# Kernel tuning notes

Measured on AMD Instinct MI355X. Metric: run time of the kernel, lower is better.

Reference implementation:

```python
import jax, jax.numpy as jnp
import numpy as np
from jax.scipy.special import erf

Z = 87
NREF = 7
NC = 5
NW = 23
N_ATOMS = 75000
N_PAIRS = 1500000
BOHR = 0.5291772105638411
HARTREE = 27.211386024367243
K4, K5, K6, KK = 4.10451, 19.08857, 254.5553148552, 7.5
E3 = float(np.exp(3.0))

def _sp_inv(x):
    # inverse of softplus, so that softplus(raw) == x
    return float(np.log(np.expm1(x)))

def compute_refc6(scale_q_raw, refsys, zeff, refh, sscale, secaiw, gam, ascale, alphaiw, hcount, cpw):
    # gather per-reference-system atomic data via refsys indices [Z, NREF]
    zeff_r = zeff[refsys][..., None]
    sscale_r = sscale[refsys][..., None]
    secaiw_r = secaiw[refsys]            # [Z, NREF, NW]
    gam_r = gam[refsys][..., None]
    refh_i = refh[..., None] * jax.nn.softplus(scale_q_raw)[0]
    qmod = zeff_r + refh_i
    qsafe = jnp.where(qmod > 1e-8, qmod, 1.0)
    zfac = jnp.where(qmod > 1e-8, jnp.exp(3.0 * (1.0 - jnp.exp(2.0 * gam_r * (1.0 - zeff_r / qsafe)))), E3)
    alpha = sscale_r * secaiw_r * zfac
    alpha = jnp.maximum(ascale[..., None] * (alphaiw - hcount[..., None] * alpha), 0.0)  # [Z, NREF, NW]
    # Casimir-Polder integration: refc6[i,j,a,b] = 3/(2pi) * sum_w alpha[i,a,w]*alpha[j,b,w]*w
    return (3.0 / (2.0 * np.pi)) * jnp.einsum('iaw,jbw,w->ijab', alpha, alpha, cpw)

def _forward(species, edge_index, lengths, partial_charges, s6_raw, s8_raw, a1_raw, a2_raw, scale_q_raw, refsys, zeff, refh, sscale, secaiw, gam, ascale, alphaiw, hcount, cpw, rcov, en, ncount_mask, ncount_weight, cn, fixgweights, refq, sqrt_r4r2):
    n = species.shape[0]
    idx_i, idx_j = edge_index[0], edge_index[1]
    r = lengths * (1.0 / BOHR)
    sp_i, sp_j = species[idx_i], species[idx_j]
    # erf-based coordination number
    rcov_ij = (4.0 / 3.0) * (rcov[sp_i] + rcov[sp_j])
    den = K4 * jnp.exp(-((jnp.abs(en[sp_i] - en[sp_j]) + K5) ** 2) / K6)
    countf = den * 0.5 * (1.0 + erf(-KK * (r - rcov_ij) / rcov_ij))
    ncoord = jax.ops.segment_sum(countf, idx_i, num_segments=n)  # [N]
    # Gaussian reference weights over (NREF, NC)
    nce = ncoord[:, None, None]
    gw = jnp.exp(-6.0 * ncount_weight[species] * (nce - cn[species]) ** 2)
    gw = jnp.sum(ncount_mask[species] * gw, axis=-1)  # [N, NREF]
    norm = jnp.clip(jnp.sum(gw, axis=-1, keepdims=True), 1e-7, None)
    gw = jnp.where(norm > 1e-8, gw / norm, fixgweights[species])
    # charge scaling zeta
    spq = jax.nn.softplus(scale_q_raw)[0]
    zeff_s = zeff[species][:, None]
    qref = zeff_s + refq[species] * spq
    qmod = zeff_s + partial_charges[:, None]
    qsafe = jnp.where(qmod > 1e-8, qmod, 1.0)
    zeta = jnp.where(qmod > 1e-8, jnp.exp(3.0 * (1.0 - jnp.exp(2.0 * gam[species][:, None] * (1.0 - qref / qsafe)))), E3) * gw  # [N, NREF]
    # pairwise C6 via reference C6 table
    refc6 = compute_refc6(scale_q_raw, refsys, zeff, refh, sscale, secaiw, gam, ascale, alphaiw, hcount, cpw)
    c6 = jnp.einsum('pab,pa,pb->p', refc6[sp_i, sp_j], zeta[idx_i], zeta[idx_j])  # [P]
    # Becke-Johnson damped -C6/r^6 - C8/r^8
    r4r2 = 3.0 * sqrt_r4r2[sp_i] * sqrt_r4r2[sp_j]
    a1 = jax.nn.softplus(a1_raw)[0]
    a2 = jax.nn.softplus(a2_raw)[0]
    s6 = jax.nn.softplus(s6_raw)[0]
    s8 = jax.nn.softplus(s8_raw)[0]
    r0sq = (a1 * jnp.sqrt(r4r2) + a2) ** 2
    r2 = r * r
    r6 = r2 * r2 * r2
    r8 = r6 * r2
    pair = -c6 * (s6 / (r6 + r0sq ** 3) + s8 * r4r2 / (r8 + r0sq ** 4))
    # per-atom dispersion energy in eV (0.5 because each pair counted twice in edge list)
    return 0.5 * HARTREE * jax.ops.segment_sum(pair, idx_i, num_segments=n)

def setup_inputs():
    key = jax.random.key(0)
    ks = jax.random.split(key, 24)
    u = lambda k, sh, lo, hi: jax.random.uniform(k, sh, jnp.float32, lo, hi)
    return {
        'species': jax.random.randint(ks[0], (N_ATOMS,), 0, Z),
        'edge_index': jax.random.randint(ks[1], (2, N_PAIRS), 0, N_ATOMS),
        'lengths': u(ks[2], (N_PAIRS,), 1.5, 6.0),
        'partial_charges': 0.1 * jax.random.normal(ks[3], (N_ATOMS,), jnp.float32),
        's6_raw': jnp.array([_sp_inv(1.0)], jnp.float32),
        's8_raw': jnp.array([_sp_inv(1.61679827)], jnp.float32),
        'a1_raw': jnp.array([_sp_inv(0.44959224)], jnp.float32),
        'a2_raw': jnp.array([_sp_inv(3.35743605)], jnp.float32),
        'scale_q_raw': jnp.array([_sp_inv(1.0)], jnp.float32),
        'refsys': jax.random.randint(ks[4], (Z, NREF), 0, Z),
        'zeff': u(ks[5], (Z,), 1.0, 10.0),
        'refh': u(ks[6], (Z, NREF), -0.5, 0.5),
        'sscale': u(ks[7], (Z,), 0.5, 1.5),
        'secaiw': u(ks[8], (Z, NW), 0.1, 5.0),
        'gam': u(ks[9], (Z,), 0.1, 0.5),
        'ascale': u(ks[10], (Z, NREF), 0.5, 1.5),
        'alphaiw': u(ks[11], (Z, NREF, NW), 0.5, 20.0),
        'hcount': u(ks[12], (Z, NREF), 0.0, 3.0),
        'cpw': u(ks[13], (NW,), 0.01, 0.5),
        'rcov': u(ks[14], (Z,), 0.5, 3.0),
        'en': u(ks[15], (Z,), 0.8, 4.0),
        'ncount_mask': (jax.random.uniform(ks[16], (Z, NREF, NC)) > 0.5).astype(jnp.float32),
        'ncount_weight': u(ks[17], (Z, NREF, NC), 0.5, 2.0),
        'cn': u(ks[18], (Z, NREF, NC), 0.0, 6.0),
        'fixgweights': jnp.full((Z, NREF), 1.0 / NREF, jnp.float32),
        'refq': u(ks[19], (Z, NREF), -0.5, 0.5),
        'sqrt_r4r2': u(ks[20], (Z,), 2.0, 10.0),
    }

def reference(species, edge_index, lengths, partial_charges, s6_raw, s8_raw, a1_raw, a2_raw, scale_q_raw, refsys, zeff, refh, sscale, secaiw, gam, ascale, alphaiw, hcount, cpw, rcov, en, ncount_mask, ncount_weight, cn, fixgweights, refq, sqrt_r4r2):
    return _forward(species, edge_index, lengths, partial_charges, s6_raw, s8_raw, a1_raw, a2_raw, scale_q_raw, refsys, zeff, refh, sscale, secaiw, gam, ascale, alphaiw, hcount, cpw, rcov, en, ncount_mask, ncount_weight, cn, fixgweights, refq, sqrt_r4r2)
```

## Files before the change

kernel.cpp:

```cpp
#include <hip/hip_runtime.h>
#include <hip/hip_bf16.h>
#include <hip/hip_fp16.h>

#define ZZ      87
#define NREF    7
#define NC      5
#define NW      23
#define NATOMS  75000
#define NPAIRS  1500000
#define IAW     (ZZ*NREF*NW)

#define BSH     7
#define BSZ     128
#define NB      586
#define BLKP    4096
#define NBLK    367
#define PREP_BLKS 147
#define PACK_BLKS 22

#define OFF_ALPHA   32
#define OFF_AD      14040
#define OFF_NCOORD  164040
#define OFF_ENERGY  239040
#define OFF_IMG     OFF_ENERGY
#define OFF_BETA    314048
#define OFF_HIST    1214048
#define OFF_BTOT    1643586
#define OFF_BBASE   1644176
#define OFF_REC     1644768
#define SORT_WS_NEED      ((size_t)(OFF_REC + 2*NPAIRS) * 4)

#define IMG_A   0
#define IMG_C   7308
#define IMG_Q   13398
#define IMG_G   14008
#define IMG_DW  14356

static constexpr float INV_BOHR  = (float)(1.0/0.5291772105638411);
static constexpr float HALF_HART = (float)(0.5*27.211386024367243);
static constexpr float CK4 = 4.10451f;
static constexpr float CK5 = 19.08857f;
static constexpr float INV_K6 = (float)(1.0/254.5553148552);
static constexpr float CKK = 7.5f;
static constexpr float E3F = 20.085536923187668f;
static constexpr float C32PI = 0.47746482927568606f;

__device__ __forceinline__ bool detect_bf16(const void* s6raw) {
    return ((*(const unsigned short*)s6raw) >> 8) == 0x3Fu;
}
__device__ __forceinline__ float ldf(const void* p, int i, bool bf) {
    if (bf) {
        unsigned int u = ((const unsigned short*)p)[i];
        return __uint_as_float(u << 16);
    }
    return ((const float*)p)[i];
}
__device__ __forceinline__ float splus(float x) {
    return (x > 15.f) ? x : log1pf(expf(x));
}
__device__ __forceinline__ void up2(unsigned int u, float* d) {
    __half2 h;
    *reinterpret_cast<unsigned int*>(&h) = u;
    float2 f = __half22float2(h);
    d[0] = f.x; d[1] = f.y;
}
__device__ __forceinline__ void unpack24(uint4 a, uint4 b, uint4 c, float* v) {
    up2(a.x, v+0);  up2(a.y, v+2);  up2(a.z, v+4);  up2(a.w, v+6);
    up2(b.x, v+8);  up2(b.y, v+10); up2(b.z, v+12); up2(b.w, v+14);
    up2(c.x, v+16); up2(c.y, v+18); up2(c.z, v+20); up2(c.w, v+22);
}
__device__ __forceinline__ void ld8(const void* p, int p0, bool bf, float* L) {
    if (bf) {
        uint4 u = *(const uint4*)((const unsigned short*)p + p0);
        unsigned vs[4] = {u.x, u.y, u.z, u.w};
        #pragma unroll
        for (int k = 0; k < 4; ++k) {
            L[2*k]   = __uint_as_float(vs[k] << 16);
            L[2*k+1] = __uint_as_float(vs[k] & 0xFFFF0000u);
        }
    } else {
        float4 f0 = *(const float4*)((const float*)p + p0);
        float4 f1 = *(const float4*)((const float*)p + p0 + 4);
        L[0]=f0.x; L[1]=f0.y; L[2]=f0.z; L[3]=f0.w;
        L[4]=f1.x; L[5]=f1.y; L[6]=f1.z; L[7]=f1.w;
    }
}

__device__ __forceinline__ void prep_body(int t, bool bf,
        const int* __restrict__ refsys, const int* __restrict__ species,
        const void* zeff, const void* refh, const void* sscale,
        const void* secaiw, const void* gam, const void* ascale,
        const void* alphaiw, const void* hcount, const void* cpw,
        const void* rcov, const void* en,
        const void* s6r, const void* s8r, const void* a1r,
        const void* a2r, const void* sqr, float* __restrict__ ws) {
    if (t == 0) {
        ws[0] = splus(ldf(sqr, 0, bf));
        ws[1] = splus(ldf(s6r, 0, bf));
        ws[2] = splus(ldf(s8r, 0, bf));
        ws[3] = splus(ldf(a1r, 0, bf));
        ws[4] = splus(ldf(a2r, 0, bf));
    }
    if (t < NATOMS) {
        int sp = species[t];
        ((float2*)(ws + OFF_AD))[t] = make_float2(ldf(rcov, sp, bf), ldf(en, sp, bf));
    }
    if (t >= IAW) return;
    int w  = t % NW;
    int ia = t / NW;
    int rs = refsys[ia];
    float spq  = splus(ldf(sqr, 0, bf));
    float ze   = ldf(zeff, rs, bf);
    float qmod = ze + ldf(refh, ia, bf) * spq;
    float zfac;
    if (qmod > 1e-8f) {
        float g = ldf(gam, rs, bf);
        zfac = expf(3.f * (1.f - expf(2.f * g * (1.f - ze / qmod))));
    } else {
        zfac = E3F;
    }
    float sec = ldf(sscale, rs, bf) * ldf(secaiw, rs*NW + w, bf) * zfac;
    float al  = ldf(ascale, ia, bf) *
                (ldf(alphaiw, ia*NW + w, bf) - ldf(hcount, ia, bf) * sec);
    float bsw = sqrtf(C32PI * ldf(cpw, w, bf));
    ws[OFF_ALPHA + t] = fmaxf(al, 0.f) * bsw;
}


__global__ __launch_bounds__(512) void k_prep_hist(
        const int* __restrict__ refsys, const int* __restrict__ species,
        const void* zeff, const void* refh, const void* sscale,
        const void* secaiw, const void* gam, const void* ascale,
        const void* alphaiw, const void* hcount, const void* cpw,
        const void* rcov, const void* en,
        const void* s6r, const void* s8r, const void* a1r,
        const void* a2r, const void* sqr,
        const int* __restrict__ eidx, int* __restrict__ hist,
        float* __restrict__ ws) {
    const bool bf = detect_bf16(s6r);
    __shared__ int h[NB];
    int blk = blockIdx.x;
    if (blk < PREP_BLKS) {
        prep_body(blk * 512 + (int)threadIdx.x, bf, refsys, species, zeff, refh,
                  sscale, secaiw, gam, ascale, alphaiw, hcount, cpw, rcov, en,
                  s6r, s8r, a1r, a2r, sqr, ws);
        return;
    }
    int hb = blk - PREP_BLKS;
    for (int t = threadIdx.x; t < NB; t += 512) h[t] = 0;
    __syncthreads();
    int p0 = hb * BLKP + (int)threadIdx.x * 8;
    if (p0 + 8 <= NPAIRS) {
        int4 a0 = *(const int4*)(eidx + p0);
        int4 a1 = *(const int4*)(eidx + p0 + 4);
        atomicAdd(&h[a0.x >> BSH], 1);
        atomicAdd(&h[a0.y >> BSH], 1);
        atomicAdd(&h[a0.z >> BSH], 1);
        atomicAdd(&h[a0.w >> BSH], 1);
        atomicAdd(&h[a1.x >> BSH], 1);
        atomicAdd(&h[a1.y >> BSH], 1);
        atomicAdd(&h[a1.z >> BSH], 1);
        atomicAdd(&h[a1.w >> BSH], 1);
    }
    __syncthreads();
    for (int t = threadIdx.x; t < NB; t += 512)
        hist[(size_t)hb * NB + t] = h[t];
}

__global__ __launch_bounds__(1024) void k_scan_bucket(int* __restrict__ hist,
                                                      int* __restrict__ btot) {
    int b = blockIdx.x;
    int t = threadIdx.x;
    int v = (t < NBLK) ? hist[(size_t)t * NB + b] : 0;
    int lane = t & 63, wid = t >> 6;
    int x = v;
    #pragma unroll
    for (int d = 1; d < 64; d <<= 1) {
        int n = __shfl_up(x, d, 64);
        if (lane >= d) x += n;
    }
    __shared__ int wsum[16];
    if (lane == 63) wsum[wid] = x;
    __syncthreads();
    if (t == 0) {
        int acc = 0;
        #pragma unroll
        for (int w = 0; w < 16; ++w) { int s = wsum[w]; wsum[w] = acc; acc += s; }
    }
    __syncthreads();
    int incl = x + wsum[wid];
    if (t < NBLK) hist[(size_t)t * NB + b] = incl - v;
    if (t == 1023) btot[b] = incl;
}

__global__ __launch_bounds__(1024) void k_scan_base(const int* __restrict__ btot,
                                                    int* __restrict__ bbase) {
    int t = threadIdx.x;
    int v = (t < NB) ? btot[t] : 0;
    int lane = t & 63, wid = t >> 6;
    int x = v;
    #pragma unroll
    for (int d = 1; d < 64; d <<= 1) {
        int n = __shfl_up(x, d, 64);
        if (lane >= d) x += n;
    }
    __shared__ int wsum[16];
    if (lane == 63) wsum[wid] = x;
    __syncthreads();
    if (t == 0) {
        int acc = 0;
        #pragma unroll
        for (int w = 0; w < 16; ++w) { int s = wsum[w]; wsum[w] = acc; acc += s; }
    }
    __syncthreads();
    int incl = x + wsum[wid];
    if (t < NB) bbase[t] = incl - v;
    if (t == 1023) bbase[NB] = incl;
}

__global__ __launch_bounds__(512) void k_scatter_pack(
        const int* __restrict__ eidx, const void* lengths, const void* s6r,
        const int* __restrict__ hist, const int* __restrict__ bbase,
        uint2* __restrict__ rec,
        const void* zeff, const void* gam, const void* mask,
        const void* wght, const void* cn, const void* refq, const void* sq4,
        float* __restrict__ ws) {
    const bool bf = detect_bf16(s6r);
    __shared__ int cnt[NB];
    int blk = blockIdx.x;
    if (blk >= NBLK) {
        unsigned* img = (unsigned*)(ws + OFF_IMG);
        int t = (blk - NBLK) * 512 + (int)threadIdx.x;
        if (t < 7308) {
            int row = t / 12, u = t % 12;
            int w0 = 2*u, w1 = 2*u + 1;
            const float* aF = ws + OFF_ALPHA + row * NW;
            float v0 = aF[w0];
            float v1 = (w1 < NW) ? aF[w1] : 0.f;
            unsigned lo = __half_as_ushort(__float2half(v0));
            unsigned hi = __half_as_ushort(__float2half(v1));
            img[t] = lo | (hi << 16);
        } else if (t < 7308 + 3045) {
            int e = t - 7308;
            float cnv = ldf(cn, e, bf);
            float wv  = (ldf(mask, e, bf) > 0.5f) ? ldf(wght, e, bf) : -1.f;
            ((float2*)(img + IMG_C))[e] = make_float2(cnv, wv);
        } else if (t < 10353 + 609) {
            int e = t - 10353;
            int sp = e / NREF;
            ((float*)(img + IMG_Q))[e] = ldf(zeff, sp, bf) + ldf(refq, e, bf) * ws[0];
        } else if (t < 10962 + 87) {
            int sp = t - 10962;
            ((float4*)(img + IMG_G))[sp] = make_float4(ldf(zeff, sp, bf),
                                                       ldf(gam, sp, bf),
                                                       ldf(sq4, sp, bf), 0.f);
        } else if (t == 11049) {
            img[14007] = 0;
        }
        return;
    }
    const int* hcol = hist + (size_t)blk * NB;
    for (int t = threadIdx.x; t < NB; t += 512)
        cnt[t] = bbase[t] + hcol[t];
    __syncthreads();
    int p0 = blk * BLKP + (int)threadIdx.x * 8;
    if (p0 + 8 > NPAIRS) return;
    int4 a0 = *(const int4*)(eidx + p0);
    int4 a1 = *(const int4*)(eidx + p0 + 4);
    int4 b0 = *(const int4*)(eidx + NPAIRS + p0);
    int4 b1 = *(const int4*)(eidx + NPAIRS + p0 + 4);
    float L[8];
    ld8(lengths, p0, bf, L);
    int is[8] = {a0.x,a0.y,a0.z,a0.w,a1.x,a1.y,a1.z,a1.w};
    int js[8] = {b0.x,b0.y,b0.z,b0.w,b1.x,b1.y,b1.z,b1.w};
    #pragma unroll
    for (int k = 0; k < 8; ++k) {
        int b = is[k] >> BSH;
        int pos = atomicAdd(&cnt[b], 1);
        rec[pos] = make_uint2(((unsigned)(is[k] & (BSZ-1)) << 17) | (unsigned)js[k],
                              __float_as_uint(L[k]));
    }
}

__global__ __launch_bounds__(512) void k_ncbeta(const uint2* __restrict__ rec,
        const int* __restrict__ bbase, const int* __restrict__ species,
        const void* pq, const void* s6r, float* __restrict__ ws) {
    const bool bf = detect_bf16(s6r);
    __shared__ __align__(16) unsigned s_img[IMG_DW];
    __shared__ float bins[BSZ];
    __shared__ float adl[BSZ * 2];
    int b = blockIdx.x;
    int a0 = b << BSH;
    int na = NATOMS - a0; if (na > BSZ) na = BSZ;
    {
        const uint4* g4 = (const uint4*)(ws + OFF_IMG);
        uint4* s4 = (uint4*)s_img;
        for (int t = threadIdx.x; t < IMG_DW/4; t += 512) s4[t] = g4[t];
    }
    for (int t = threadIdx.x; t < BSZ; t += 512) bins[t] = 0.f;
    const float2* AD = (const float2*)(ws + OFF_AD);
    for (int t = threadIdx.x; t < na; t += 512) {
        float2 v = AD[a0 + t];
        adl[2*t] = v.x; adl[2*t + 1] = v.y;
    }
    __syncthreads();
    int bs = bbase[b], be = bbase[b + 1];
    for (int p = bs + (int)threadIdx.x; p < be; p += 2*512) {
        int p2 = p + 512;
        bool h2 = (p2 < be);
        uint2 r1 = rec[p];
        uint2 r2 = h2 ? rec[p2] : r1;
        int il1 = (r1.x >> 17) & (BSZ-1), j1 = r1.x & 0x1FFFF;
        int il2 = (r2.x >> 17) & (BSZ-1), j2 = r2.x & 0x1FFFF;
        float2 aj1 = AD[j1];
        float2 aj2 = AD[j2];
        {
            float r  = __uint_as_float(r1.y) * INV_BOHR;
            float rc = (4.f/3.f) * (adl[2*il1] + aj1.x);
            float d  = fabsf(adl[2*il1+1] - aj1.y) + CK5;
            float cf = CK4 * expf(-(d*d)*INV_K6) * 0.5f * (1.f + erff(-CKK*(r-rc)/rc));
            atomicAdd(&bins[il1], cf);
        }
        if (h2) {
            float r  = __uint_as_float(r2.y) * INV_BOHR;
            float rc = (4.f/3.f) * (adl[2*il2] + aj2.x);
            float d  = fabsf(adl[2*il2+1] - aj2.y) + CK5;
            float cf = CK4 * expf(-(d*d)*INV_K6) * 0.5f * (1.f + erff(-CKK*(r-rc)/rc));
            atomicAdd(&bins[il2], cf);
        }
    }
    __syncthreads();
    int t = threadIdx.x;
    if (t >= na) return;
    int k = a0 + t;
    const unsigned* sA = s_img;
    const float2*   sC = (const float2*)(s_img + IMG_C);
    const float*    sQ = (const float*)(s_img + IMG_Q);
    const float4*   sG = (const float4*)(s_img + IMG_G);

    int sp = species[k];
    float nce = bins[t];
    float4 zg = sG[sp];
    float qmod = zg.x + ldf(pq, k, bf);

    float gw[NREF];
    float sum = 0.f;
    #pragma unroll
    for (int a = 0; a < NREF; ++a) {
        float g = 0.f;
        #pragma unroll
        for (int c = 0; c < NC; ++c) {
            float2 cw = sC[sp*35 + a*NC + c];
            float dlt = nce - cw.x;
            float e = __expf(-6.f * cw.y * dlt * dlt);
            g += (cw.y > 0.f) ? e : 0.f;
        }
        gw[a] = g; sum += g;
    }
    float inv = 1.f / fmaxf(sum, 1e-7f);

    float2 acc[12];
    #pragma unroll
    for (int u = 0; u < 12; ++u) acc[u] = make_float2(0.f, 0.f);
    #pragma unroll
    for (int a = 0; a < NREF; ++a) {
        float qref = sQ[sp*NREF + a];
        float zf = (qmod > 1e-8f)
                 ? __expf(3.f * (1.f - __expf(2.f * zg.y * (1.f - qref / qmod))))
                 : E3F;
        float za = zf * gw[a] * inv;
        const uint2* ar = (const uint2*)(sA + (sp*NREF + a) * 12);
        #pragma unroll
        for (int u2 = 0; u2 < 6; ++u2) {
            uint2 h = ar[u2];
            float f[4];
            up2(h.x, f); up2(h.y, f+2);
            acc[2*u2].x   = fmaf(f[0], za, acc[2*u2].x);
            acc[2*u2].y   = fmaf(f[1], za, acc[2*u2].y);
            acc[2*u2+1].x = fmaf(f[2], za, acc[2*u2+1].x);
            acc[2*u2+1].y = fmaf(f[3], za, acc[2*u2+1].y);
        }
    }
    alignas(16) __half hrow[24];
    #pragma unroll
    for (int u = 0; u < 12; ++u) {
        hrow[2*u]   = __float2half(acc[u].x);
        hrow[2*u+1] = __float2half(acc[u].y);
    }
    hrow[23] = __float2half(zg.z);
    uint4* dst = (uint4*)((char*)(ws + OFF_BETA) + (size_t)k * 48);
    const uint4* src = (const uint4*)hrow;
    dst[0] = src[0]; dst[1] = src[1]; dst[2] = src[2];
}

__device__ __forceinline__ float pair_energy(const float* vi, const float* vj,
                                             float len, float s6, float s8,
                                             float a1, float a2) {
    float c6 = 0.f;
    #pragma unroll
    for (int w = 0; w < NW; ++w) c6 = fmaf(vi[w], vj[w], c6);
    float rr = 3.f * vi[23] * vj[23];
    float r  = len * INV_BOHR;
    float r2 = r * r;
    float r6 = r2 * r2 * r2;
    float r8 = r6 * r2;
    float r0   = a1 * sqrtf(rr) + a2;
    float r0sq = r0 * r0;
    float r0_6 = r0sq * r0sq * r0sq;
    float r0_8 = r0_6 * r0sq;
    return -c6 * (s6 / (r6 + r0_6) + s8 * rr / (r8 + r0_8));
}

__global__ __launch_bounds__(512) void k_energy_s(const uint2* __restrict__ rec,
        const int* __restrict__ bbase, const float* __restrict__ ws,
        void* __restrict__ out, const void* s6r) {
    const bool bf = detect_bf16(s6r);
    __shared__ float bins[BSZ];
    __shared__ unsigned irow[BSZ * 13];
    int b = blockIdx.x;
    int a0 = b << BSH;
    int na = NATOMS - a0; if (na > BSZ) na = BSZ;
    for (int t = threadIdx.x; t < BSZ; t += 512) bins[t] = 0.f;
    const unsigned* betaU = (const unsigned*)(ws + OFF_BETA);
    for (int t = threadIdx.x; t < na * 12; t += 512) {
        int l = t / 12, k = t - l * 12;
        irow[l * 13 + k] = betaU[(size_t)(a0 + l) * 12 + k];
    }
    __syncthreads();
    float s6 = ws[1], s8 = ws[2], a1 = ws[3], a2 = ws[4];
    int bs = bbase[b], be = bbase[b + 1];
    const char* B = (const char*)betaU;
    for (int p = bs + (int)threadIdx.x; p < be; p += 2*512) {
        int p2 = p + 512;
        bool h2 = (p2 < be);
        uint2 r1 = rec[p];
        uint2 r2 = h2 ? rec[p2] : r1;
        int il1 = (r1.x >> 17) & (BSZ-1), j1 = r1.x & 0x1FFFF;
        int il2 = (r2.x >> 17) & (BSZ-1), j2 = r2.x & 0x1FFFF;
        const uint4* J1 = (const uint4*)(B + (size_t)j1 * 48);
        const uint4* J2 = (const uint4*)(B + (size_t)j2 * 48);
        uint4 ja0 = J1[0], ja1 = J1[1], ja2 = J1[2];
        uint4 jb0 = J2[0], jb1 = J2[1], jb2 = J2[2];
        float vi[24], vj[24];
        #pragma unroll
        for (int k = 0; k < 12; ++k) up2(irow[il1*13 + k], vi + 2*k);
        unpack24(ja0, ja1, ja2, vj);
        float e1 = pair_energy(vi, vj, __uint_as_float(r1.y), s6, s8, a1, a2);
        atomicAdd(&bins[il1], e1);
        if (h2) {
            #pragma unroll
            for (int k = 0; k < 12; ++k) up2(irow[il2*13 + k], vi + 2*k);
            unpack24(jb0, jb1, jb2, vj);
            float e2 = pair_energy(vi, vj, __uint_as_float(r2.y), s6, s8, a1, a2);
            atomicAdd(&bins[il2], e2);
        }
    }
    __syncthreads();
    for (int t = threadIdx.x; t < na; t += 512) {
        float v = HALF_HART * bins[t];
        if (bf) ((__hip_bfloat16*)out)[a0 + t] = __float2bfloat16(v);
        else    ((float*)out)[a0 + t] = v;
    }
}


__global__ void k_prep_fb(const int* __restrict__ refsys, const int* __restrict__ species,
                          const void* zeff, const void* refh, const void* sscale,
                          const void* secaiw, const void* gam, const void* ascale,
                          const void* alphaiw, const void* hcount, const void* cpw,
                          const void* rcov, const void* en,
                          const void* s6r, const void* s8r, const void* a1r,
                          const void* a2r, const void* sqr,
                          float* __restrict__ ws) {
    const bool bf = detect_bf16(s6r);
    prep_body(blockIdx.x * blockDim.x + threadIdx.x, bf, refsys, species, zeff,
              refh, sscale, secaiw, gam, ascale, alphaiw, hcount, cpw, rcov, en,
              s6r, s8r, a1r, a2r, sqr, ws);
}

__device__ __forceinline__ float2 ldf2(const void* p, int t, bool bf) {
    if (bf) {
        unsigned int u = ((const unsigned int*)p)[t];
        return make_float2(__uint_as_float(u << 16),
                           __uint_as_float(u & 0xFFFF0000u));
    }
    return ((const float2*)p)[t];
}

__global__ void k_ncoord_fb(const int* __restrict__ eidx, const void* lengths,
                            const void* s6r, float* __restrict__ ws) {
    const bool bf = detect_bf16(s6r);
    int t = blockIdx.x * blockDim.x + threadIdx.x;
    if (2*t >= NPAIRS) return;
    int2 ii = ((const int2*)eidx)[t];
    int2 jj = ((const int2*)(eidx + NPAIRS))[t];
    float2 L = ldf2(lengths, t, bf);
    const float2* AD = (const float2*)(ws + OFF_AD);
    float2 ai = AD[ii.x], aj = AD[jj.x];
    float2 bi = AD[ii.y], bj = AD[jj.y];
    float r0  = L.x * INV_BOHR;
    float rc0 = (4.f/3.f) * (ai.x + aj.x);
    float d0  = fabsf(ai.y - aj.y) + CK5;
    float cf0 = CK4 * expf(-(d0*d0) * INV_K6) * 0.5f * (1.f + erff(-CKK * (r0 - rc0) / rc0));
    float r1  = L.y * INV_BOHR;
    float rc1 = (4.f/3.f) * (bi.x + bj.x);
    float d1  = fabsf(bi.y - bj.y) + CK5;
    float cf1 = CK4 * expf(-(d1*d1) * INV_K6) * 0.5f * (1.f + erff(-CKK * (r1 - rc1) / rc1));
    atomicAdd(ws + OFF_NCOORD + ii.x, cf0);
    atomicAdd(ws + OFF_NCOORD + ii.y, cf1);
}

__global__ void k_beta_fb(const int* __restrict__ species, const void* pq,
                          const void* zeff, const void* gam,
                          const void* mask, const void* wght, const void* cn,
                          const void* refq, const void* sq4, const void* s6r,
                          float* __restrict__ ws) {
    const bool bf = detect_bf16(s6r);
    int k = blockIdx.x * blockDim.x + threadIdx.x;
    if (k >= NATOMS) return;
    int sp = species[k];
    float nce = ws[OFF_NCOORD + k];
    float spq = ws[0];
    float gw[NREF];
    float sum = 0.f;
    #pragma unroll
    for (int a = 0; a < NREF; ++a) {
        float g = 0.f;
        #pragma unroll
        for (int c = 0; c < NC; ++c) {
            int idx = (sp*NREF + a)*NC + c;
            float dlt = nce - ldf(cn, idx, bf);
            g += ldf(mask, idx, bf) * expf(-6.f * ldf(wght, idx, bf) * dlt * dlt);
        }
        gw[a] = g; sum += g;
    }
    float inv  = 1.f / fmaxf(sum, 1e-7f);
    float ze   = ldf(zeff, sp, bf);
    float qmod = ze + ldf(pq, k, bf);
    float gm   = ldf(gam, sp, bf);
    float beta[NW];
    #pragma unroll
    for (int w = 0; w < NW; ++w) beta[w] = 0.f;
    const float* A = ws + OFF_ALPHA + sp * (NREF*NW);
    #pragma unroll
    for (int a = 0; a < NREF; ++a) {
        float qref = ze + ldf(refq, sp*NREF + a, bf) * spq;
        float zf = (qmod > 1e-8f)
                 ? expf(3.f * (1.f - expf(2.f * gm * (1.f - qref / qmod))))
                 : E3F;
        float za = zf * gw[a] * inv;
        #pragma unroll
        for (int w = 0; w < NW; ++w) beta[w] = fmaf(A[a*NW + w], za, beta[w]);
    }
    alignas(16) __half hrow[24];
    #pragma unroll
    for (int w = 0; w < NW; ++w) hrow[w] = __float2half(beta[w]);
    hrow[23] = __float2half(ldf(sq4, sp, bf));
    uint4* dst = (uint4*)((char*)(ws + OFF_BETA) + (size_t)k * 48);
    const uint4* src = (const uint4*)hrow;
    dst[0] = src[0]; dst[1] = src[1]; dst[2] = src[2];
}

__global__ void k_energy_fb(const int* __restrict__ eidx, const void* lengths,
                            const void* s6r, float* __restrict__ ws) {
    const bool bf = detect_bf16(s6r);
    int t = blockIdx.x * blockDim.x + threadIdx.x;
    if (2*t >= NPAIRS) return;
    int2 ii = ((const int2*)eidx)[t];
    int2 jj = ((const int2*)(eidx + NPAIRS))[t];
    float2 L = ldf2(lengths, t, bf);
    const char* B = (const char*)(ws + OFF_BETA);
    const uint4* qi0 = (const uint4*)(B + (size_t)ii.x * 48);
    const uint4* qj0 = (const uint4*)(B + (size_t)jj.x * 48);
    const uint4* qi1 = (const uint4*)(B + (size_t)ii.y * 48);
    const uint4* qj1 = (const uint4*)(B + (size_t)jj.y * 48);
    uint4 ra0 = qi0[0], ra1 = qi0[1], ra2 = qi0[2];
    uint4 rb0 = qj0[0], rb1 = qj0[1], rb2 = qj0[2];
    uint4 rc0 = qi1[0], rc1 = qi1[1], rc2 = qi1[2];
    uint4 rd0 = qj1[0], rd1 = qj1[1], rd2 = qj1[2];
    float s6 = ws[1], s8 = ws[2], a1 = ws[3], a2 = ws[4];
    float vi[24], vj[24];
    unpack24(ra0, ra1, ra2, vi);
    unpack24(rb0, rb1, rb2, vj);
    float e0 = pair_energy(vi, vj, L.x, s6, s8, a1, a2);
    unpack24(rc0, rc1, rc2, vi);
    unpack24(rd0, rd1, rd2, vj);
    float e1 = pair_energy(vi, vj, L.y, s6, s8, a1, a2);
    atomicAdd(ws + OFF_ENERGY + ii.x, e0);
    atomicAdd(ws + OFF_ENERGY + ii.y, e1);
}

__global__ void k_final(const float* __restrict__ ws, void* out, const void* s6r) {
    const bool bf = detect_bf16(s6r);
    int k = blockIdx.x * blockDim.x + threadIdx.x;
    if (k >= NATOMS) return;
    float v = HALF_HART * ws[OFF_ENERGY + k];
    if (bf) ((__hip_bfloat16*)out)[k] = __float2bfloat16(v);
    else    ((float*)out)[k] = v;
}

extern "C" void kernel_launch(void* const* d_in, const int* in_sizes, int n_in,
                              void* d_out, int out_size, void* d_ws, size_t ws_size,
                              hipStream_t stream) {
    (void)in_sizes; (void)n_in; (void)out_size;

    const int*  species = (const int*)d_in[0];
    const int*  eidx    = (const int*)d_in[1];
    const void* lengths = d_in[2];
    const void* pq      = d_in[3];
    const void* s6r     = d_in[4];
    const void* s8r     = d_in[5];
    const void* a1r     = d_in[6];
    const void* a2r     = d_in[7];
    const void* sqr     = d_in[8];
    const int*  refsys  = (const int*)d_in[9];
    const void* zeff    = d_in[10];
    const void* refh    = d_in[11];
    const void* sscale  = d_in[12];
    const void* secaiw  = d_in[13];
    const void* gam     = d_in[14];
    const void* ascale  = d_in[15];
    const void* alphaiw = d_in[16];
    const void* hcount  = d_in[17];
    const void* cpw     = d_in[18];
    const void* rcov    = d_in[19];
    const void* en      = d_in[20];
    const void* mask    = d_in[21];
    const void* wght    = d_in[22];
    const void* cn      = d_in[23];
    const void* refq    = d_in[25];
    const void* sq4     = d_in[26];

    float* ws = (float*)d_ws;
    const bool use_sort = (ws_size >= SORT_WS_NEED);

    if (use_sort) {
        int*   hist  = (int*)(ws + OFF_HIST);
        int*   btot  = (int*)(ws + OFF_BTOT);
        int*   bbase = (int*)(ws + OFF_BBASE);
        uint2* rec   = (uint2*)(ws + OFF_REC);

        k_prep_hist  <<<PREP_BLKS + NBLK, 512, 0, stream>>>(refsys, species,
                         zeff, refh, sscale, secaiw, gam, ascale, alphaiw,
                         hcount, cpw, rcov, en, s6r, s8r, a1r, a2r, sqr,
                         eidx, hist, ws);
        k_scan_bucket<<<NB, 1024, 0, stream>>>(hist, btot);
        k_scan_base  <<<1,  1024, 0, stream>>>(btot, bbase);
        k_scatter_pack<<<NBLK + PACK_BLKS, 512, 0, stream>>>(eidx, lengths, s6r,
                         hist, bbase, rec, zeff, gam, mask, wght, cn, refq,
                         sq4, ws);
        k_ncbeta     <<<NB, 512, 0, stream>>>(rec, bbase, species, pq, s6r, ws);
        k_energy_s   <<<NB, 512, 0, stream>>>(rec, bbase, ws, d_out, s6r);
    } else {
        hipMemsetAsync(ws + OFF_NCOORD, 0, (size_t)(2 * NATOMS) * sizeof(float), stream);
        k_prep_fb  <<<(NATOMS   + 511)/512, 512, 0, stream>>>(refsys, species,
                        zeff, refh, sscale, secaiw, gam, ascale, alphaiw,
                        hcount, cpw, rcov, en, s6r, s8r, a1r, a2r, sqr, ws);
        k_ncoord_fb<<<(NPAIRS/2 + 255)/256, 256, 0, stream>>>(eidx, lengths, s6r, ws);
        k_beta_fb  <<<(NATOMS   + 255)/256, 256, 0, stream>>>(species, pq, zeff, gam,
                        mask, wght, cn, refq, sq4, s6r, ws);
        k_energy_fb<<<(NPAIRS/2 + 255)/256, 256, 0, stream>>>(eidx, lengths, s6r, ws);
        k_final    <<<(NATOMS   + 255)/256, 256, 0, stream>>>(ws, d_out, s6r);
    }
}
```

Measured before the change: 75.38 us.

## Fuse bucket and base scans via last-block ticket, move prep into scan kernel

```diff
diff --git a/kernel.cpp b/kernel.cpp
--- a/kernel.cpp
+++ b/kernel.cpp
@@ -15,9 +15,10 @@
 #define NB      586
 #define BLKP    4096
 #define NBLK    367
-#define PREP_BLKS 147
+#define PREPB   74
 #define PACK_BLKS 22
 
+#define OFF_DONE    8
 #define OFF_ALPHA   32
 #define OFF_AD      14040
 #define OFF_NCOORD  164040
@@ -127,29 +128,15 @@
 }
 
 
-__global__ __launch_bounds__(512) void k_prep_hist(
-        const int* __restrict__ refsys, const int* __restrict__ species,
-        const void* zeff, const void* refh, const void* sscale,
-        const void* secaiw, const void* gam, const void* ascale,
-        const void* alphaiw, const void* hcount, const void* cpw,
-        const void* rcov, const void* en,
-        const void* s6r, const void* s8r, const void* a1r,
-        const void* a2r, const void* sqr,
-        const int* __restrict__ eidx, int* __restrict__ hist,
-        float* __restrict__ ws) {
-    const bool bf = detect_bf16(s6r);
+__global__ __launch_bounds__(512) void k_hist(const int* __restrict__ eidx,
+                                              int* __restrict__ hist,
+                                              float* __restrict__ ws) {
     __shared__ int h[NB];
     int blk = blockIdx.x;
-    if (blk < PREP_BLKS) {
-        prep_body(blk * 512 + (int)threadIdx.x, bf, refsys, species, zeff, refh,
-                  sscale, secaiw, gam, ascale, alphaiw, hcount, cpw, rcov, en,
-                  s6r, s8r, a1r, a2r, sqr, ws);
-        return;
-    }
-    int hb = blk - PREP_BLKS;
+    if (blk == 0 && threadIdx.x == 0) ((int*)ws)[OFF_DONE] = 0;
     for (int t = threadIdx.x; t < NB; t += 512) h[t] = 0;
     __syncthreads();
-    int p0 = hb * BLKP + (int)threadIdx.x * 8;
+    int p0 = blk * BLKP + (int)threadIdx.x * 8;
     if (p0 + 8 <= NPAIRS) {
         int4 a0 = *(const int4*)(eidx + p0);
         int4 a1 = *(const int4*)(eidx + p0 + 4);
@@ -164,13 +151,31 @@
     }
     __syncthreads();
     for (int t = threadIdx.x; t < NB; t += 512)
-        hist[(size_t)hb * NB + t] = h[t];
-}
-
-__global__ __launch_bounds__(1024) void k_scan_bucket(int* __restrict__ hist,
-                                                      int* __restrict__ btot) {
-    int b = blockIdx.x;
+        hist[(size_t)blk * NB + t] = h[t];
+}
+
+__global__ __launch_bounds__(1024) void k_scan_prep(
+        int* __restrict__ hist, int* __restrict__ btot, int* __restrict__ bbase,
+        const int* __restrict__ refsys, const int* __restrict__ species,
+        const void* zeff, const void* refh, const void* sscale,
+        const void* secaiw, const void* gam, const void* ascale,
+        const void* alphaiw, const void* hcount, const void* cpw,
+        const void* rcov, const void* en,
+        const void* s6r, const void* s8r, const void* a1r,
+        const void* a2r, const void* sqr,
+        float* __restrict__ ws) {
+    const bool bf = detect_bf16(s6r);
+    int blk = blockIdx.x;
+    if (blk >= NB) {
+        prep_body((blk - NB) * 1024 + (int)threadIdx.x, bf, refsys, species,
+                  zeff, refh, sscale, secaiw, gam, ascale, alphaiw, hcount,
+                  cpw, rcov, en, s6r, s8r, a1r, a2r, sqr, ws);
+        return;
+    }
+    int b = blk;
     int t = threadIdx.x;
+    __shared__ int wsum[16];
+    __shared__ int sTicket;
     int v = (t < NBLK) ? hist[(size_t)t * NB + b] : 0;
     int lane = t & 63, wid = t >> 6;
     int x = v;
@@ -179,7 +184,6 @@
         int n = __shfl_up(x, d, 64);
         if (lane >= d) x += n;
     }
-    __shared__ int wsum[16];
     if (lane == 63) wsum[wid] = x;
     __syncthreads();
     if (t == 0) {
@@ -190,22 +194,22 @@
     __syncthreads();
     int incl = x + wsum[wid];
     if (t < NBLK) hist[(size_t)t * NB + b] = incl - v;
-    if (t == 1023) btot[b] = incl;
-}
-
-__global__ __launch_bounds__(1024) void k_scan_base(const int* __restrict__ btot,
-                                                    int* __restrict__ bbase) {
-    int t = threadIdx.x;
-    int v = (t < NB) ? btot[t] : 0;
-    int lane = t & 63, wid = t >> 6;
-    int x = v;
+    if (t == 1023) {
+        btot[b] = incl;
+        __threadfence();
+        sTicket = atomicAdd((int*)ws + OFF_DONE, 1);
+    }
+    __syncthreads();
+    if (sTicket != NB - 1) return;
+    __threadfence();
+    int v2 = (t < NB) ? atomicAdd(&btot[t], 0) : 0;
+    int x2 = v2;
     #pragma unroll
     for (int d = 1; d < 64; d <<= 1) {
-        int n = __shfl_up(x, d, 64);
-        if (lane >= d) x += n;
-    }
-    __shared__ int wsum[16];
-    if (lane == 63) wsum[wid] = x;
+        int n = __shfl_up(x2, d, 64);
+        if (lane >= d) x2 += n;
+    }
+    if (lane == 63) wsum[wid] = x2;
     __syncthreads();
     if (t == 0) {
         int acc = 0;
@@ -213,9 +217,9 @@
         for (int w = 0; w < 16; ++w) { int s = wsum[w]; wsum[w] = acc; acc += s; }
     }
     __syncthreads();
-    int incl = x + wsum[wid];
-    if (t < NB) bbase[t] = incl - v;
-    if (t == 1023) bbase[NB] = incl;
+    int incl2 = x2 + wsum[wid];
+    if (t < NB) bbase[t] = incl2 - v2;
+    if (t == 1023) bbase[NB] = incl2;
 }
 
 __global__ __launch_bounds__(512) void k_scatter_pack(
@@ -640,17 +644,16 @@
         int*   bbase = (int*)(ws + OFF_BBASE);
         uint2* rec   = (uint2*)(ws + OFF_REC);
 
-        k_prep_hist  <<<PREP_BLKS + NBLK, 512, 0, stream>>>(refsys, species,
-                         zeff, refh, sscale, secaiw, gam, ascale, alphaiw,
-                         hcount, cpw, rcov, en, s6r, s8r, a1r, a2r, sqr,
-                         eidx, hist, ws);
-        k_scan_bucket<<<NB, 1024, 0, stream>>>(hist, btot);
-        k_scan_base  <<<1,  1024, 0, stream>>>(btot, bbase);
+        k_hist        <<<NBLK, 512, 0, stream>>>(eidx, hist, ws);
+        k_scan_prep   <<<NB + PREPB, 1024, 0, stream>>>(hist, btot, bbase,
+                          refsys, species, zeff, refh, sscale, secaiw, gam,
+                          ascale, alphaiw, hcount, cpw, rcov, en,
+                          s6r, s8r, a1r, a2r, sqr, ws);
         k_scatter_pack<<<NBLK + PACK_BLKS, 512, 0, stream>>>(eidx, lengths, s6r,
-                         hist, bbase, rec, zeff, gam, mask, wght, cn, refq,
-                         sq4, ws);
-        k_ncbeta     <<<NB, 512, 0, stream>>>(rec, bbase, species, pq, s6r, ws);
-        k_energy_s   <<<NB, 512, 0, stream>>>(rec, bbase, ws, d_out, s6r);
+                          hist, bbase, rec, zeff, gam, mask, wght, cn, refq,
+                          sq4, ws);
+        k_ncbeta      <<<NB, 512, 0, stream>>>(rec, bbase, species, pq, s6r, ws);
+        k_energy_s    <<<NB, 512, 0, stream>>>(rec, bbase, ws, d_out, s6r);
     } else {
         hipMemsetAsync(ws + OFF_NCOORD, 0, (size_t)(2 * NATOMS) * sizeof(float), stream);
         k_prep_fb  <<<(NATOMS   + 511)/512, 512, 0, stream>>>(refsys, species,
```

New measurement: 101.0 us (median of 2 runs). 34.0% more time.
